# Kernel tuning notes

Measured on AMD Instinct MI355X. Metric: run time of the kernel, lower is better.

Reference implementation:

```python
import jax, jax.numpy as jnp
import numpy as np
from jax.scipy.linalg import expm

B = 16384
K = 64          # number of subgroups
M = 6           # mat_dim per subgroup (subgroup_size = 36)
NUM_ACTIONS = 16


def setup_inputs() -> dict:
    key = jax.random.key(0)
    k1, k2, k3, k4 = jax.random.split(key, 4)
    group_feats = jax.random.normal(k1, (B, K * M * M), dtype=jnp.float32)
    act = jax.random.randint(k2, (B,), 0, NUM_ACTIONS)
    act_params = jax.random.normal(k3, (NUM_ACTIONS, K), dtype=jnp.float32) * 0.001
    lie_alg_basis = jax.random.normal(k4, (K, M, M), dtype=jnp.float32)
    return {"group_feats": group_feats, "act": act,
            "act_params": act_params, "lie_alg_basis": lie_alg_basis}


def reference(group_feats, act, act_params, lie_alg_basis):
    # apply_act: act_repr = blockdiag_k expm(a_{bk} * (L_k - L_k^T)); out = act_repr @ blockdiag(group_feats)
    sel = act_params[act]                                   # [B, K]  (index_select on act_params)
    skew = lie_alg_basis - jnp.swapaxes(lie_alg_basis, -2, -1)  # [K, M, M]
    lie_alg = sel[:, :, None, None] * skew[None]            # [B, K, M, M]
    # batched matrix exponential over all B*K small blocks
    lie_group = jax.vmap(expm)(lie_alg.reshape(-1, M, M)).reshape(B, K, M, M)
    gf_mat = group_feats.reshape(B, K, M, M)                # to_group_matrix (block-diag blocks)
    # block-diagonal matmul == full dense matmul since off-diagonal blocks are zero
    post = jnp.einsum('bkij,bkjl->bkil', lie_group, gf_mat)
    return post.reshape(B, K * M * M)                       # to_group_feats
```

## Files before the change

kernel.cpp:

```cpp
#include <hip/hip_runtime.h>
#include <stdint.h>

#define BATCH 16384
#define KSUB 64
#define MDIM 6
#define MM 36
#define NACT 16
#define F4PB 9
#define WGT 64

typedef float f32x4 __attribute__((ext_vector_type(4)));

__global__ void expm_table_kernel(const float* __restrict__ act_params,
                                  const float* __restrict__ basis,
                                  float* __restrict__ Rtab)
{
    int gid = blockIdx.x * blockDim.x + threadIdx.x;
    if (gid >= NACT * KSUB) return;
    int a = gid / KSUB;
    int k = gid - a * KSUB;

    float L[MM];
#pragma unroll
    for (int i = 0; i < MM; ++i) L[i] = basis[k * MM + i];
    float p = act_params[a * KSUB + k];

    float A[MM];
#pragma unroll
    for (int i = 0; i < MDIM; ++i)
#pragma unroll
        for (int j = 0; j < MDIM; ++j)
            A[i * MDIM + j] = p * (L[i * MDIM + j] - L[j * MDIM + i]);

    float E[MM], T[MM];
#pragma unroll
    for (int i = 0; i < MM; ++i) { E[i] = 0.f; T[i] = 0.f; }
#pragma unroll
    for (int i = 0; i < MDIM; ++i) { E[i * MDIM + i] = 1.f; T[i * MDIM + i] = 1.f; }

    for (int n = 1; n <= 10; ++n) {
        float Tn[MM];
        float inv = 1.0f / (float)n;
#pragma unroll
        for (int i = 0; i < MDIM; ++i)
#pragma unroll
            for (int l = 0; l < MDIM; ++l) {
                float s = 0.f;
#pragma unroll
                for (int j = 0; j < MDIM; ++j)
                    s += A[i * MDIM + j] * T[j * MDIM + l];
                Tn[i * MDIM + l] = s * inv;
            }
#pragma unroll
        for (int i = 0; i < MM; ++i) { T[i] = Tn[i]; E[i] += Tn[i]; }
    }
#pragma unroll
    for (int i = 0; i < MM; ++i) Rtab[gid * MM + i] = E[i];
}

__global__ __launch_bounds__(WGT, 4) void apply_kernel(
    const f32x4* __restrict__ gf4,
    const int* __restrict__ act,
    const float* __restrict__ Rtab,
    f32x4* __restrict__ out4)
{
    __shared__ f32x4 lds4[WGT * F4PB];
    const int tid = threadIdx.x;
    const int b = blockIdx.x;
    const size_t base4 = (size_t)b * (WGT * F4PB);

#pragma unroll
    for (int i = 0; i < F4PB; ++i) {
        __builtin_amdgcn_global_load_lds(
            (const __attribute__((address_space(1))) uint32_t*)(gf4 + base4 + (i << 6) + tid),
            (__attribute__((address_space(3))) uint32_t*)(&lds4[i << 6]),
            16, 0, 0);
    }

    const int a = act[b];
    const f32x4* R4 = (const f32x4*)(Rtab + (size_t)((a << 6) + tid) * MM);
    float R[MM];
#pragma unroll
    for (int q = 0; q < F4PB; ++q) {
        f32x4 rv = R4[q];
        R[4 * q + 0] = rv.x; R[4 * q + 1] = rv.y;
        R[4 * q + 2] = rv.z; R[4 * q + 3] = rv.w;
    }

    __syncthreads();

    const f32x4* grow4 = (const f32x4*)(&lds4[tid * F4PB]);
    float O[MM];
#pragma unroll
    for (int q = 0; q < F4PB; ++q) {
        f32x4 g = grow4[q];
#pragma unroll
        for (int e = 0; e < 4; ++e) {
            const int idx = 4 * q + e;
            const int j = idx / MDIM;
            const int l = idx - j * MDIM;
            const float gv = g[e];
#pragma unroll
            for (int i = 0; i < MDIM; ++i) {
                if (idx < MDIM)
                    O[i * MDIM + l] = R[i * MDIM + 0] * gv;
                else
                    O[i * MDIM + l] = fmaf(R[i * MDIM + j], gv, O[i * MDIM + l]);
            }
        }
    }

    f32x4* orow = (f32x4*)(&lds4[tid * F4PB]);
#pragma unroll
    for (int q = 0; q < F4PB; ++q) {
        f32x4 v;
        v.x = O[4 * q + 0]; v.y = O[4 * q + 1];
        v.z = O[4 * q + 2]; v.w = O[4 * q + 3];
        orow[q] = v;
    }
    __syncthreads();

#pragma unroll
    for (int i = 0; i < F4PB; ++i) {
        int p4 = (i << 6) + tid;
        __builtin_nontemporal_store(lds4[p4], &out4[base4 + p4]);
    }
}

extern "C" void kernel_launch(void* const* d_in, const int* in_sizes, int n_in,
                              void* d_out, int out_size, void* d_ws, size_t ws_size,
                              hipStream_t stream) {
    const float* gf    = (const float*)d_in[0];
    const int*   act   = (const int*)d_in[1];
    const float* ap    = (const float*)d_in[2];
    const float* basis = (const float*)d_in[3];

    float* Rtab = (float*)d_ws;

    expm_table_kernel<<<16, 64, 0, stream>>>(ap, basis, Rtab);

    apply_kernel<<<BATCH, WGT, 0, stream>>>((const f32x4*)gf, act, Rtab,
                                            (f32x4*)d_out);
}
```

Baseline: 276.1 us.

## Split each 6x6 block across two threads and store output directly

The apply kernel now uses 128 threads per batch row, with two threads per subgroup, each computing three output rows of the 6x6 product. Input is loaded with nontemporal vector loads into LDS instead of global_load_lds. Each thread writes its 18 results straight to global memory as float2 stores, which drops the second LDS staging pass and barrier. This adds parallelism and cuts per-thread registers, but the float2 stores are strided by 36 floats per thread and may coalesce less well than the old contiguous float4 stores.

Result: slower. 338.8 us (+22.7%).

```diff
diff --git a/kernel.cpp b/kernel.cpp
--- a/kernel.cpp
+++ b/kernel.cpp
@@ -7,9 +7,10 @@
 #define MM 36
 #define NACT 16
 #define F4PB 9
-#define WGT 64
+#define WGT 128
 
 typedef float f32x4 __attribute__((ext_vector_type(4)));
+typedef float f32x2 __attribute__((ext_vector_type(2)));
 
 __global__ void expm_table_kernel(const float* __restrict__ act_params,
                                   const float* __restrict__ basis,
@@ -58,42 +59,46 @@
     for (int i = 0; i < MM; ++i) Rtab[gid * MM + i] = E[i];
 }
 
-__global__ __launch_bounds__(WGT, 4) void apply_kernel(
+__global__ __launch_bounds__(WGT, 8) void apply_kernel(
     const f32x4* __restrict__ gf4,
     const int* __restrict__ act,
     const float* __restrict__ Rtab,
-    f32x4* __restrict__ out4)
+    float* __restrict__ outf)
 {
-    __shared__ f32x4 lds4[WGT * F4PB];
+    __shared__ f32x4 lds4[KSUB * F4PB];
     const int tid = threadIdx.x;
     const int b = blockIdx.x;
-    const size_t base4 = (size_t)b * (WGT * F4PB);
-
-#pragma unroll
-    for (int i = 0; i < F4PB; ++i) {
-        __builtin_amdgcn_global_load_lds(
-            (const __attribute__((address_space(1))) uint32_t*)(gf4 + base4 + (i << 6) + tid),
-            (__attribute__((address_space(3))) uint32_t*)(&lds4[i << 6]),
-            16, 0, 0);
-    }
+    const int k = tid >> 1;
+    const int h = tid & 1;
+    const size_t base4 = (size_t)b * (KSUB * F4PB);
 
     const int a = act[b];
-    const f32x4* R4 = (const f32x4*)(Rtab + (size_t)((a << 6) + tid) * MM);
-    float R[MM];
+    const f32x2* R2 = (const f32x2*)(Rtab + (size_t)((a << 6) + k) * MM + 18 * h);
+    f32x2 r2[9];
 #pragma unroll
-    for (int q = 0; q < F4PB; ++q) {
-        f32x4 rv = R4[q];
-        R[4 * q + 0] = rv.x; R[4 * q + 1] = rv.y;
-        R[4 * q + 2] = rv.z; R[4 * q + 3] = rv.w;
-    }
+    for (int m = 0; m < 9; ++m) r2[m] = R2[m];
+
+    f32x4 sv[4];
+#pragma unroll
+    for (int i = 0; i < 4; ++i)
+        sv[i] = __builtin_nontemporal_load(&gf4[base4 + tid + (i << 7)]);
+    f32x4 st;
+    if (tid < 64) st = __builtin_nontemporal_load(&gf4[base4 + 512 + tid]);
+#pragma unroll
+    for (int i = 0; i < 4; ++i) lds4[tid + (i << 7)] = sv[i];
+    if (tid < 64) lds4[512 + tid] = st;
+
+    float R[18];
+#pragma unroll
+    for (int m = 0; m < 9; ++m) { R[2 * m] = r2[m].x; R[2 * m + 1] = r2[m].y; }
 
     __syncthreads();
 
-    const f32x4* grow4 = (const f32x4*)(&lds4[tid * F4PB]);
-    float O[MM];
+    const f32x4* grow = &lds4[k * F4PB];
+    float O[18];
 #pragma unroll
     for (int q = 0; q < F4PB; ++q) {
-        f32x4 g = grow4[q];
+        f32x4 g = grow[q];
 #pragma unroll
         for (int e = 0; e < 4; ++e) {
             const int idx = 4 * q + e;
@@ -101,29 +106,20 @@
             const int l = idx - j * MDIM;
             const float gv = g[e];
 #pragma unroll
-            for (int i = 0; i < MDIM; ++i) {
+            for (int i = 0; i < 3; ++i) {
                 if (idx < MDIM)
-                    O[i * MDIM + l] = R[i * MDIM + 0] * gv;
+                    O[i * MDIM + l] = R[i * MDIM] * gv;
                 else
                     O[i * MDIM + l] = fmaf(R[i * MDIM + j], gv, O[i * MDIM + l]);
             }
         }
     }
 
-    f32x4* orow = (f32x4*)(&lds4[tid * F4PB]);
+    f32x2* o2 = (f32x2*)(outf + (size_t)b * (KSUB * MM) + k * MM + 18 * h);
 #pragma unroll
-    for (int q = 0; q < F4PB; ++q) {
-        f32x4 v;
-        v.x = O[4 * q + 0]; v.y = O[4 * q + 1];
-        v.z = O[4 * q + 2]; v.w = O[4 * q + 3];
-        orow[q] = v;
-    }
-    __syncthreads();
-
-#pragma unroll
-    for (int i = 0; i < F4PB; ++i) {
-        int p4 = (i << 6) + tid;
-        __builtin_nontemporal_store(lds4[p4], &out4[base4 + p4]);
+    for (int m = 0; m < 9; ++m) {
+        f32x2 v; v.x = O[2 * m]; v.y = O[2 * m + 1];
+        __builtin_nontemporal_store(v, &o2[m]);
     }
 }
 
@@ -140,5 +136,5 @@
     expm_table_kernel<<<16, 64, 0, stream>>>(ap, basis, Rtab);
 
     apply_kernel<<<BATCH, WGT, 0, stream>>>((const f32x4*)gf, act, Rtab,
-                                            (f32x4*)d_out);
+                                            (float*)d_out);
 }
```
